# Optimization experiments

Measured on AMD Instinct MI355X. Metric: run time of the kernel, lower is better.

Reference implementation:

```python
import jax, jax.numpy as jnp
import numpy as np

N_NODES = 50000
N_EDGES = 800000
N_LABEL = 200000
IN_C, HID_C, OUT_C = 128, 128, 64


def setup_inputs() -> dict:
    key = jax.random.key(0)
    ks = jax.random.split(key, 9)
    s = lambda fan_in: 1.0 / np.sqrt(fan_in)
    return {
        "x": jax.random.normal(ks[0], (N_NODES, IN_C), jnp.float32),
        "W1": jax.random.normal(ks[1], (IN_C, HID_C), jnp.float32) * s(IN_C),
        "b1": jnp.zeros((HID_C,), jnp.float32),
        "W2": jax.random.normal(ks[2], (HID_C, HID_C), jnp.float32) * s(HID_C),
        "b2": jnp.zeros((HID_C,), jnp.float32),
        "W3": jax.random.normal(ks[3], (HID_C, OUT_C), jnp.float32) * s(HID_C),
        "b3": jnp.zeros((OUT_C,), jnp.float32),
        "edge_index": jax.random.randint(ks[4], (2, N_EDGES), 0, N_NODES, jnp.int32),
        "edge_label_index": jax.random.randint(ks[5], (2, N_LABEL), 0, N_NODES, jnp.int32),
    }


def _gcn_conv(x, W, b, src, dst, dinv, num_nodes):
    # x @ W then symmetric-normalized scatter-sum over edges (self-loops included in src/dst)
    h = x @ W                                  # [N, out]
    norm = dinv[src] * dinv[dst]               # [E+N]
    msgs = h[src] * norm[:, None]              # [E+N, out]
    out = jax.ops.segment_sum(msgs, dst, num_segments=num_nodes)
    return out + b


def _encode(x, W1, b1, W2, b2, W3, b3, edge_index, num_nodes):
    loops = jnp.arange(num_nodes, dtype=edge_index.dtype)
    src = jnp.concatenate([edge_index[0], loops])
    dst = jnp.concatenate([edge_index[1], loops])
    # degree (with self-loops) at targets; deg >= 1 so rsqrt is safe
    deg = jax.ops.segment_sum(jnp.ones(dst.shape[0], x.dtype), dst, num_segments=num_nodes)
    dinv = jax.lax.rsqrt(deg)
    z = _gcn_conv(x, W1, b1, src, dst, dinv, num_nodes)
    z = jax.nn.relu(z)  # dropout treated as eval-mode identity
    z = _gcn_conv(z, W2, b2, src, dst, dinv, num_nodes)
    z = jax.nn.relu(z)
    z = _gcn_conv(z, W3, b3, src, dst, dinv, num_nodes)
    return z


def reference(x, W1, b1, W2, b2, W3, b3, edge_index, edge_label_index):
    z = _encode(x, W1, b1, W2, b2, W3, b3, edge_index, N_NODES)
    # decode: gather both endpoints, elementwise mul, sum over feature dim
    return (z[edge_label_index[0]] * z[edge_label_index[1]]).sum(axis=-1)
```

## Files before the change

kernel.cpp:

```cpp
#include <hip/hip_runtime.h>

#define N_NODES 50000
#define N_EDGES 800000
#define N_LABEL 200000
#define ROW_BLOCKS 782

typedef __attribute__((ext_vector_type(4))) float f32x4;
typedef _Float16 f16;
typedef __attribute__((ext_vector_type(8))) _Float16 f16x8;

__global__ __launch_bounds__(256)
void k_zero(int4* __restrict__ p, int n4) {
    int i = blockIdx.x * 256 + threadIdx.x;
    if (i < n4) p[i] = int4{0, 0, 0, 0};
}

__global__ __launch_bounds__(256)
void k_prep(const float* __restrict__ W1, const float* __restrict__ W2,
            const float* __restrict__ W3,
            f16* WT1h, f16* WT1l, f16* WT2h, f16* WT2l, f16* WT3h, f16* WT3l,
            const int* __restrict__ dst, int* cnt) {
    int b = blockIdx.x, tid = threadIdx.x;
    if (b < 64) {
        int t = b * 256 + tid;
        int c = t >> 7, k = t & 127;
        float w = W1[k * 128 + c];
        f16 h = (f16)w;
        WT1h[c * 128 + k] = h; WT1l[c * 128 + k] = (f16)(w - (float)h);
        w = W2[k * 128 + c];
        h = (f16)w;
        WT2h[c * 128 + k] = h; WT2l[c * 128 + k] = (f16)(w - (float)h);
        if (c < 64) {
            w = W3[k * 64 + c];
            h = (f16)w;
            WT3h[c * 128 + k] = h; WT3l[c * 128 + k] = (f16)(w - (float)h);
        }
    } else {
        int vb = b - 64;
        int g = vb & 7;
        int i = (vb >> 3) * 256 + tid;
        int d = dst[i];
        if ((unsigned)(d - g * 6250) < 6250u) atomicAdd(&cnt[d], 1);
    }
}

__global__ __launch_bounds__(256)
void k_partial(const int* __restrict__ cnt, float* __restrict__ dinv,
               int* __restrict__ bsum, int N) {
    __shared__ int wsum[4];
    int b = blockIdx.x, t = threadIdx.x;
    int i = b * 256 + t;
    int v = (i < N) ? cnt[i] : 0;
    if (i < N) dinv[i] = rsqrtf((float)v + 1.0f);
    int s = v;
#pragma unroll
    for (int d = 1; d < 64; d <<= 1) s += __shfl_xor(s, d, 64);
    if ((t & 63) == 0) wsum[t >> 6] = s;
    __syncthreads();
    if (t == 0) bsum[b] = wsum[0] + wsum[1] + wsum[2] + wsum[3];
}

__global__ __launch_bounds__(256)
void k_offsets(const int* __restrict__ cnt, const int* __restrict__ bsum,
               int* __restrict__ off, int N, int NB) {
    __shared__ int wsum[4];
    __shared__ int add0_s;
    int b = blockIdx.x, t = threadIdx.x;
    int v0 = (t < b && t < NB) ? bsum[t] : 0;
    int s0 = v0;
#pragma unroll
    for (int d = 1; d < 64; d <<= 1) s0 += __shfl_xor(s0, d, 64);
    if ((t & 63) == 0) wsum[t >> 6] = s0;
    __syncthreads();
    if (t == 0) add0_s = wsum[0] + wsum[1] + wsum[2] + wsum[3];
    __syncthreads();
    int add = add0_s;
    __syncthreads();
    int i = b * 256 + t;
    int v = (i < N) ? cnt[i] : 0;
    int lane = t & 63, w = t >> 6;
    int sv = v;
#pragma unroll
    for (int d = 1; d < 64; d <<= 1) {
        int u = __shfl_up(sv, d, 64);
        if (lane >= d) sv += u;
    }
    if (lane == 63) wsum[w] = sv;
    __syncthreads();
    for (int ww = 0; ww < w; ++ww) add += wsum[ww];
    if (i < N) off[i + 1] = add + sv;
    if (i == 0) off[0] = 0;
}

__global__ __launch_bounds__(256)
void k_bucket(const int* __restrict__ srcv, const int* __restrict__ dstv,
              const int* __restrict__ off, int* cnt2, unsigned short* __restrict__ csr) {
    int vb = blockIdx.x;
    int g = vb & 7;
    int i = (vb >> 3) * 256 + threadIdx.x;
    int d = dstv[i];
    if ((unsigned)(d - g * 6250) < 6250u) {
        int slot = off[d] + atomicAdd(&cnt2[d], 1);
        csr[slot] = (unsigned short)srcv[i];
    }
}

__global__ __launch_bounds__(256)
void k_gemm1(const float* __restrict__ x,
             const f16* __restrict__ WTh, const f16* __restrict__ WTl,
             const float* __restrict__ dinv, f16* __restrict__ A, int N) {
    constexpr int M = 128, NCB = 4;
    __shared__ f16 Hs[64 * 136];
    __shared__ f16 Ls[64 * 136];
    int b = blockIdx.x;
    int c0 = (b & 1) * 64;
    int t = threadIdx.x;

#pragma unroll
    for (int i = 0; i < 4; ++i) {
        int ch = t + i * 256;
        int col = ch >> 4;
        int kc = (ch & 15) * 8;
        *(f16x8*)&Hs[col * 136 + kc] = *(const f16x8*)&WTh[(long)(c0 + col) * 128 + kc];
        *(f16x8*)&Ls[col * 136 + kc] = *(const f16x8*)&WTl[(long)(c0 + col) * 128 + kc];
    }

    int wv = t >> 6, l = t & 63;
    int r0w = (b >> 1) * 64 + wv * 16;
    int arow = r0w + (l & 15);
    if (arow >= N) arow = N - 1;
    int kb = (l >> 4) * 8;

    f16x8 ah[4], al[4];
#pragma unroll
    for (int ks = 0; ks < 4; ++ks) {
        const float* xp = &x[(long)arow * 128 + ks * 32 + kb];
        float4 a0 = *(const float4*)xp;
        float4 a1 = *(const float4*)(xp + 4);
        float fv[8] = {a0.x, a0.y, a0.z, a0.w, a1.x, a1.y, a1.z, a1.w};
#pragma unroll
        for (int j = 0; j < 8; ++j) {
            f16 h = (f16)fv[j];
            ah[ks][j] = h;
            al[ks][j] = (f16)(fv[j] - (float)h);
        }
    }
    __syncthreads();

    f32x4 acc[NCB];
#pragma unroll
    for (int cb = 0; cb < NCB; ++cb) acc[cb] = f32x4{0.f, 0.f, 0.f, 0.f};
#pragma unroll
    for (int ks = 0; ks < 4; ++ks) {
#pragma unroll
        for (int cb = 0; cb < NCB; ++cb) {
            int wi = (cb * 16 + (l & 15)) * 136 + ks * 32 + kb;
            f16x8 bh = *(const f16x8*)&Hs[wi];
            f16x8 bl = *(const f16x8*)&Ls[wi];
            acc[cb] = __builtin_amdgcn_mfma_f32_16x16x32_f16(ah[ks], bh, acc[cb], 0, 0, 0);
            acc[cb] = __builtin_amdgcn_mfma_f32_16x16x32_f16(ah[ks], bl, acc[cb], 0, 0, 0);
            acc[cb] = __builtin_amdgcn_mfma_f32_16x16x32_f16(al[ks], bh, acc[cb], 0, 0, 0);
        }
    }
    int rbase = r0w + (l >> 4) * 4;
    float dv[4];
#pragma unroll
    for (int i = 0; i < 4; ++i) dv[i] = (rbase + i < N) ? dinv[rbase + i] : 0.f;
#pragma unroll
    for (int cb = 0; cb < NCB; ++cb) {
#pragma unroll
        for (int i = 0; i < 4; ++i) {
            int r = rbase + i;
            if (r < N) A[(long)r * M + c0 + cb * 16 + (l & 15)] = (f16)(acc[cb][i] * dv[i]);
        }
    }
}

template<int M>
__global__ __launch_bounds__(256)
void k_gemm23(const f16* __restrict__ B,
              const f16* __restrict__ WTh, const f16* __restrict__ WTl,
              const float* __restrict__ dinv, f16* __restrict__ A, int N) {
    constexpr int NCB = M / 32;
    constexpr int HC = M / 2;
    __shared__ f16 Hs[HC * 136];
    __shared__ f16 Ls[HC * 136];
    int b = blockIdx.x;
    int c0 = (b & 1) * HC;
    int t = threadIdx.x;

#pragma unroll
    for (int i = 0; i < HC / 16; ++i) {
        int ch = t + i * 256;
        int col = ch >> 4;
        int kc = (ch & 15) * 8;
        *(f16x8*)&Hs[col * 136 + kc] = *(const f16x8*)&WTh[(long)(c0 + col) * 128 + kc];
        *(f16x8*)&Ls[col * 136 + kc] = *(const f16x8*)&WTl[(long)(c0 + col) * 128 + kc];
    }

    int wv = t >> 6, l = t & 63;
    int r0w = (b >> 1) * 64 + wv * 16;
    int arow = r0w + (l & 15);
    if (arow >= N) arow = N - 1;
    int kb = (l >> 4) * 8;

    f16x8 a[4];
#pragma unroll
    for (int ks = 0; ks < 4; ++ks)
        a[ks] = *(const f16x8*)&B[(long)arow * 128 + ks * 32 + kb];
    __syncthreads();

    f32x4 acc[NCB];
#pragma unroll
    for (int cb = 0; cb < NCB; ++cb) acc[cb] = f32x4{0.f, 0.f, 0.f, 0.f};
#pragma unroll
    for (int ks = 0; ks < 4; ++ks) {
#pragma unroll
        for (int cb = 0; cb < NCB; ++cb) {
            int wi = (cb * 16 + (l & 15)) * 136 + ks * 32 + kb;
            f16x8 bh = *(const f16x8*)&Hs[wi];
            f16x8 bl = *(const f16x8*)&Ls[wi];
            acc[cb] = __builtin_amdgcn_mfma_f32_16x16x32_f16(a[ks], bh, acc[cb], 0, 0, 0);
            acc[cb] = __builtin_amdgcn_mfma_f32_16x16x32_f16(a[ks], bl, acc[cb], 0, 0, 0);
        }
    }
    int rbase = r0w + (l >> 4) * 4;
    float dv[4];
#pragma unroll
    for (int i = 0; i < 4; ++i) dv[i] = (rbase + i < N) ? dinv[rbase + i] : 0.f;
#pragma unroll
    for (int cb = 0; cb < NCB; ++cb) {
#pragma unroll
        for (int i = 0; i < 4; ++i) {
            int r = rbase + i;
            if (r < N) A[(long)r * M + c0 + cb * 16 + (l & 15)] = (f16)(acc[cb][i] * dv[i]);
        }
    }
}

__global__ __launch_bounds__(256)
void k_gather(const f16* __restrict__ A, const int* __restrict__ off,
              const unsigned short* __restrict__ csr, const float* __restrict__ dinv,
              const float* __restrict__ bias, float* __restrict__ Bf,
              f16* __restrict__ Bo,
              int N, int M, int lg, int relu, int mode) {
    int t = blockIdx.x * blockDim.x + threadIdx.x;
    int node = t >> lg;
    if (node >= N) return;
    int q = (t & ((1 << lg) - 1)) << 3;
    const f16* Aq = A + q;

    float acc[8];
    {
        f16x8 v = *(const f16x8*)&Aq[(long)node * M];
#pragma unroll
        for (int c = 0; c < 8; ++c) acc[c] = (float)v[c];
    }
    int j = off[node], j1 = off[node + 1];
    for (; j + 8 <= j1; j += 8) {
        int s0 = csr[j + 0], s1 = csr[j + 1], s2 = csr[j + 2], s3 = csr[j + 3];
        int s4 = csr[j + 4], s5 = csr[j + 5], s6 = csr[j + 6], s7 = csr[j + 7];
        f16x8 v0 = *(const f16x8*)&Aq[(long)s0 * M];
        f16x8 v1 = *(const f16x8*)&Aq[(long)s1 * M];
        f16x8 v2 = *(const f16x8*)&Aq[(long)s2 * M];
        f16x8 v3 = *(const f16x8*)&Aq[(long)s3 * M];
        f16x8 v4 = *(const f16x8*)&Aq[(long)s4 * M];
        f16x8 v5 = *(const f16x8*)&Aq[(long)s5 * M];
        f16x8 v6 = *(const f16x8*)&Aq[(long)s6 * M];
        f16x8 v7 = *(const f16x8*)&Aq[(long)s7 * M];
#pragma unroll
        for (int c = 0; c < 8; ++c)
            acc[c] += ((float)v0[c] + (float)v1[c] + (float)v2[c] + (float)v3[c])
                    + ((float)v4[c] + (float)v5[c] + (float)v6[c] + (float)v7[c]);
    }
    for (; j + 2 <= j1; j += 2) {
        int s0 = csr[j + 0], s1 = csr[j + 1];
        f16x8 v0 = *(const f16x8*)&Aq[(long)s0 * M];
        f16x8 v1 = *(const f16x8*)&Aq[(long)s1 * M];
#pragma unroll
        for (int c = 0; c < 8; ++c) acc[c] += (float)v0[c] + (float)v1[c];
    }
    if (j < j1) {
        int s = csr[j];
        f16x8 v = *(const f16x8*)&Aq[(long)s * M];
#pragma unroll
        for (int c = 0; c < 8; ++c) acc[c] += (float)v[c];
    }

    float sc = dinv[node];
    float4 bb0 = *(const float4*)&bias[q];
    float4 bb1 = *(const float4*)&bias[q + 4];
    float bv[8] = {bb0.x, bb0.y, bb0.z, bb0.w, bb1.x, bb1.y, bb1.z, bb1.w};
#pragma unroll
    for (int c = 0; c < 8; ++c) {
        acc[c] = acc[c] * sc + bv[c];
        if (relu) acc[c] = fmaxf(acc[c], 0.f);
    }
    if (mode == 0) {
        float4 o0 = make_float4(acc[0], acc[1], acc[2], acc[3]);
        float4 o1 = make_float4(acc[4], acc[5], acc[6], acc[7]);
        *(float4*)&Bf[(long)node * M + q] = o0;
        *(float4*)&Bf[(long)node * M + q + 4] = o1;
    } else {
        f16x8 o;
#pragma unroll
        for (int c = 0; c < 8; ++c) o[c] = (f16)acc[c];
        *(f16x8*)&Bo[(long)node * M + q] = o;
    }
}

__global__ void k_decode(const float* __restrict__ z, const int* __restrict__ eli,
                         float* __restrict__ out, int L) {
    int t = blockIdx.x * blockDim.x + threadIdx.x;
    int e = t >> 4;
    int lane = t & 15;
    if (e >= L) return;
    int a = eli[e], b = eli[L + e];
    float4 va = *(const float4*)&z[(long)a * 64 + lane * 4];
    float4 vb = *(const float4*)&z[(long)b * 64 + lane * 4];
    float s = va.x * vb.x + va.y * vb.y + va.z * vb.z + va.w * vb.w;
    s += __shfl_xor(s, 1, 16);
    s += __shfl_xor(s, 2, 16);
    s += __shfl_xor(s, 4, 16);
    s += __shfl_xor(s, 8, 16);
    if (lane == 0) out[e] = s;
}

extern "C" void kernel_launch(void* const* d_in, const int* in_sizes, int n_in,
                              void* d_out, int out_size, void* d_ws, size_t ws_size,
                              hipStream_t stream) {
    const float* x   = (const float*)d_in[0];
    const float* W1  = (const float*)d_in[1];
    const float* b1  = (const float*)d_in[2];
    const float* W2  = (const float*)d_in[3];
    const float* b2  = (const float*)d_in[4];
    const float* W3  = (const float*)d_in[5];
    const float* b3  = (const float*)d_in[6];
    const int*   ei  = (const int*)d_in[7];
    const int*   eli = (const int*)d_in[8];
    float* out = (float*)d_out;

    char* ws = (char*)d_ws;
    float* dinv = (float*)ws;                  ws += 50048 * 4;
    f16*   A    = (f16*)ws;                    ws += (long)N_NODES * 128 * 2;
    f16*   B    = (f16*)ws;                    ws += (long)N_NODES * 128 * 2;
    float* z    = (float*)ws;                  ws += (long)N_NODES * 64 * 4;
    int*   cnt  = (int*)ws;                    ws += 50048 * 4;
    int*   cnt2 = (int*)ws;                    ws += 50048 * 4;
    int*   off  = (int*)ws;                    ws += 50048 * 4;
    unsigned short* csr = (unsigned short*)ws; ws += (long)N_EDGES * 2;
    int*   bsum = (int*)ws;                    ws += 256 * 4;
    f16*   WT1h = (f16*)ws;                    ws += 16384 * 2;
    f16*   WT1l = (f16*)ws;                    ws += 16384 * 2;
    f16*   WT2h = (f16*)ws;                    ws += 16384 * 2;
    f16*   WT2l = (f16*)ws;                    ws += 16384 * 2;
    f16*   WT3h = (f16*)ws;                    ws += 8192 * 2;
    f16*   WT3l = (f16*)ws;                    ws += 8192 * 2;

    const int* esrc = ei;
    const int* edst = ei + N_EDGES;

    const int NB = (N_NODES + 255) / 256;

    k_zero   <<<98, 256, 0, stream>>>((int4*)cnt, 25024);
    k_prep   <<<25064, 256, 0, stream>>>(W1, W2, W3, WT1h, WT1l, WT2h, WT2l,
                                         WT3h, WT3l, edst, cnt);
    k_partial<<<NB, 256, 0, stream>>>(cnt, dinv, bsum, N_NODES);
    k_offsets<<<NB, 256, 0, stream>>>(cnt, bsum, off, N_NODES, NB);
    k_bucket <<<25000, 256, 0, stream>>>(esrc, edst, off, cnt2, csr);

    const int ga128 = (N_NODES * 16 + 255) / 256;
    const int ga64  = (N_NODES * 8 + 255) / 256;

    k_gemm1<<<ROW_BLOCKS * 2, 256, 0, stream>>>(x, WT1h, WT1l, dinv, A, N_NODES);
    k_gather<<<ga128, 256, 0, stream>>>(A, off, csr, dinv, b1, nullptr, B,
                                        N_NODES, 128, 4, 1, 1);
    k_gemm23<128><<<ROW_BLOCKS * 2, 256, 0, stream>>>(B, WT2h, WT2l, dinv, A, N_NODES);
    k_gather<<<ga128, 256, 0, stream>>>(A, off, csr, dinv, b2, nullptr, B,
                                        N_NODES, 128, 4, 1, 1);
    k_gemm23<64><<<ROW_BLOCKS * 2, 256, 0, stream>>>(B, WT3h, WT3l, dinv, A, N_NODES);
    k_gather<<<ga64, 256, 0, stream>>>(A, off, csr, dinv, b3, z, nullptr,
                                       N_NODES, 64, 3, 0, 0);

    k_decode<<<(N_LABEL * 16 + 255) / 256, 256, 0, stream>>>(z, eli, out, N_LABEL);
}
```

Before: 216.8 us.

## Partition gather and decode work by XCD column slices for L2 locality

Gather kernels are specialized to fixed widths and remap block indices so each group of blocks (blockIdx mod 8) handles one column slice of the feature matrix and one node range. With round-robin block dispatch across XCDs, each XCD's L2 then only needs to cache a fraction of the gathered rows. Decode is likewise split into per-column-slice partial dot products written to a scratch buffer, then reduced by a second kernel. This adds an extra kernel launch and a 3.2 MB scratch buffer, and it relies on the hardware's block-to-XCD scheduling.

New measurement: 247.3 us. +14.0%, slower.

```diff
diff --git a/kernel.cpp b/kernel.cpp
--- a/kernel.cpp
+++ b/kernel.cpp
@@ -239,20 +239,21 @@
 }
 
 __global__ __launch_bounds__(256)
-void k_gather(const f16* __restrict__ A, const int* __restrict__ off,
-              const unsigned short* __restrict__ csr, const float* __restrict__ dinv,
-              const float* __restrict__ bias, float* __restrict__ Bf,
-              f16* __restrict__ Bo,
-              int N, int M, int lg, int relu, int mode) {
-    int t = blockIdx.x * blockDim.x + threadIdx.x;
-    int node = t >> lg;
-    if (node >= N) return;
-    int q = (t & ((1 << lg) - 1)) << 3;
+void k_gather128(const f16* __restrict__ A, const int* __restrict__ off,
+                 const unsigned short* __restrict__ csr, const float* __restrict__ dinv,
+                 const float* __restrict__ bias, f16* __restrict__ Bo) {
+    int vb = blockIdx.x;
+    int g = vb & 7, blk = vb >> 3;
+    int t = threadIdx.x;
+    int nl = blk * 64 + (t >> 2);
+    if (nl >= 25000) return;
+    int node = (g & 1) * 25000 + nl;
+    int q = (g >> 1) * 32 + (t & 3) * 8;
     const f16* Aq = A + q;
 
     float acc[8];
     {
-        f16x8 v = *(const f16x8*)&Aq[(long)node * M];
+        f16x8 v = *(const f16x8*)&Aq[(long)node * 128];
 #pragma unroll
         for (int c = 0; c < 8; ++c) acc[c] = (float)v[c];
     }
@@ -260,14 +261,14 @@
     for (; j + 8 <= j1; j += 8) {
         int s0 = csr[j + 0], s1 = csr[j + 1], s2 = csr[j + 2], s3 = csr[j + 3];
         int s4 = csr[j + 4], s5 = csr[j + 5], s6 = csr[j + 6], s7 = csr[j + 7];
-        f16x8 v0 = *(const f16x8*)&Aq[(long)s0 * M];
-        f16x8 v1 = *(const f16x8*)&Aq[(long)s1 * M];
-        f16x8 v2 = *(const f16x8*)&Aq[(long)s2 * M];
-        f16x8 v3 = *(const f16x8*)&Aq[(long)s3 * M];
-        f16x8 v4 = *(const f16x8*)&Aq[(long)s4 * M];
-        f16x8 v5 = *(const f16x8*)&Aq[(long)s5 * M];
-        f16x8 v6 = *(const f16x8*)&Aq[(long)s6 * M];
-        f16x8 v7 = *(const f16x8*)&Aq[(long)s7 * M];
+        f16x8 v0 = *(const f16x8*)&Aq[(long)s0 * 128];
+        f16x8 v1 = *(const f16x8*)&Aq[(long)s1 * 128];
+        f16x8 v2 = *(const f16x8*)&Aq[(long)s2 * 128];
+        f16x8 v3 = *(const f16x8*)&Aq[(long)s3 * 128];
+        f16x8 v4 = *(const f16x8*)&Aq[(long)s4 * 128];
+        f16x8 v5 = *(const f16x8*)&Aq[(long)s5 * 128];
+        f16x8 v6 = *(const f16x8*)&Aq[(long)s6 * 128];
+        f16x8 v7 = *(const f16x8*)&Aq[(long)s7 * 128];
 #pragma unroll
         for (int c = 0; c < 8; ++c)
             acc[c] += ((float)v0[c] + (float)v1[c] + (float)v2[c] + (float)v3[c])
@@ -275,55 +276,114 @@
     }
     for (; j + 2 <= j1; j += 2) {
         int s0 = csr[j + 0], s1 = csr[j + 1];
-        f16x8 v0 = *(const f16x8*)&Aq[(long)s0 * M];
-        f16x8 v1 = *(const f16x8*)&Aq[(long)s1 * M];
+        f16x8 v0 = *(const f16x8*)&Aq[(long)s0 * 128];
+        f16x8 v1 = *(const f16x8*)&Aq[(long)s1 * 128];
 #pragma unroll
         for (int c = 0; c < 8; ++c) acc[c] += (float)v0[c] + (float)v1[c];
     }
     if (j < j1) {
         int s = csr[j];
-        f16x8 v = *(const f16x8*)&Aq[(long)s * M];
+        f16x8 v = *(const f16x8*)&Aq[(long)s * 128];
 #pragma unroll
         for (int c = 0; c < 8; ++c) acc[c] += (float)v[c];
     }
-
     float sc = dinv[node];
     float4 bb0 = *(const float4*)&bias[q];
     float4 bb1 = *(const float4*)&bias[q + 4];
     float bv[8] = {bb0.x, bb0.y, bb0.z, bb0.w, bb1.x, bb1.y, bb1.z, bb1.w};
-#pragma unroll
-    for (int c = 0; c < 8; ++c) {
-        acc[c] = acc[c] * sc + bv[c];
-        if (relu) acc[c] = fmaxf(acc[c], 0.f);
-    }
-    if (mode == 0) {
-        float4 o0 = make_float4(acc[0], acc[1], acc[2], acc[3]);
-        float4 o1 = make_float4(acc[4], acc[5], acc[6], acc[7]);
-        *(float4*)&Bf[(long)node * M + q] = o0;
-        *(float4*)&Bf[(long)node * M + q + 4] = o1;
-    } else {
-        f16x8 o;
-#pragma unroll
-        for (int c = 0; c < 8; ++c) o[c] = (f16)acc[c];
-        *(f16x8*)&Bo[(long)node * M + q] = o;
-    }
-}
-
-__global__ void k_decode(const float* __restrict__ z, const int* __restrict__ eli,
-                         float* __restrict__ out, int L) {
-    int t = blockIdx.x * blockDim.x + threadIdx.x;
-    int e = t >> 4;
-    int lane = t & 15;
-    if (e >= L) return;
-    int a = eli[e], b = eli[L + e];
-    float4 va = *(const float4*)&z[(long)a * 64 + lane * 4];
-    float4 vb = *(const float4*)&z[(long)b * 64 + lane * 4];
-    float s = va.x * vb.x + va.y * vb.y + va.z * vb.z + va.w * vb.w;
-    s += __shfl_xor(s, 1, 16);
-    s += __shfl_xor(s, 2, 16);
-    s += __shfl_xor(s, 4, 16);
-    s += __shfl_xor(s, 8, 16);
-    if (lane == 0) out[e] = s;
+    f16x8 o;
+#pragma unroll
+    for (int c = 0; c < 8; ++c) o[c] = (f16)fmaxf(acc[c] * sc + bv[c], 0.f);
+    *(f16x8*)&Bo[(long)node * 128 + q] = o;
+}
+
+__global__ __launch_bounds__(256)
+void k_gather64(const f16* __restrict__ A, const int* __restrict__ off,
+                const unsigned short* __restrict__ csr, const float* __restrict__ dinv,
+                const float* __restrict__ bias, float* __restrict__ z) {
+    int vb = blockIdx.x;
+    int g = vb & 7, blk = vb >> 3;
+    int t = threadIdx.x;
+    int nl = blk * 64 + (t >> 2);
+    if (nl >= 12500) return;
+    int node = (g >> 1) * 12500 + nl;
+    int q = (g & 1) * 32 + (t & 3) * 8;
+    const f16* Aq = A + q;
+
+    float acc[8];
+    {
+        f16x8 v = *(const f16x8*)&Aq[(long)node * 64];
+#pragma unroll
+        for (int c = 0; c < 8; ++c) acc[c] = (float)v[c];
+    }
+    int j = off[node], j1 = off[node + 1];
+    for (; j + 8 <= j1; j += 8) {
+        int s0 = csr[j + 0], s1 = csr[j + 1], s2 = csr[j + 2], s3 = csr[j + 3];
+        int s4 = csr[j + 4], s5 = csr[j + 5], s6 = csr[j + 6], s7 = csr[j + 7];
+        f16x8 v0 = *(const f16x8*)&Aq[(long)s0 * 64];
+        f16x8 v1 = *(const f16x8*)&Aq[(long)s1 * 64];
+        f16x8 v2 = *(const f16x8*)&Aq[(long)s2 * 64];
+        f16x8 v3 = *(const f16x8*)&Aq[(long)s3 * 64];
+        f16x8 v4 = *(const f16x8*)&Aq[(long)s4 * 64];
+        f16x8 v5 = *(const f16x8*)&Aq[(long)s5 * 64];
+        f16x8 v6 = *(const f16x8*)&Aq[(long)s6 * 64];
+        f16x8 v7 = *(const f16x8*)&Aq[(long)s7 * 64];
+#pragma unroll
+        for (int c = 0; c < 8; ++c)
+            acc[c] += ((float)v0[c] + (float)v1[c] + (float)v2[c] + (float)v3[c])
+                    + ((float)v4[c] + (float)v5[c] + (float)v6[c] + (float)v7[c]);
+    }
+    for (; j + 2 <= j1; j += 2) {
+        int s0 = csr[j + 0], s1 = csr[j + 1];
+        f16x8 v0 = *(const f16x8*)&Aq[(long)s0 * 64];
+        f16x8 v1 = *(const f16x8*)&Aq[(long)s1 * 64];
+#pragma unroll
+        for (int c = 0; c < 8; ++c) acc[c] += (float)v0[c] + (float)v1[c];
+    }
+    if (j < j1) {
+        int s = csr[j];
+        f16x8 v = *(const f16x8*)&Aq[(long)s * 64];
+#pragma unroll
+        for (int c = 0; c < 8; ++c) acc[c] += (float)v[c];
+    }
+    float sc = dinv[node];
+    float4 bb0 = *(const float4*)&bias[q];
+    float4 bb1 = *(const float4*)&bias[q + 4];
+    float4 o0, o1;
+    o0.x = acc[0] * sc + bb0.x; o0.y = acc[1] * sc + bb0.y;
+    o0.z = acc[2] * sc + bb0.z; o0.w = acc[3] * sc + bb0.w;
+    o1.x = acc[4] * sc + bb1.x; o1.y = acc[5] * sc + bb1.y;
+    o1.z = acc[6] * sc + bb1.z; o1.w = acc[7] * sc + bb1.w;
+    *(float4*)&z[(long)node * 64 + q] = o0;
+    *(float4*)&z[(long)node * 64 + q + 4] = o1;
+}
+
+__global__ __launch_bounds__(256)
+void k_decode_part(const float* __restrict__ z, const int* __restrict__ eli,
+                   float* __restrict__ P) {
+    int vb = blockIdx.x;
+    int g = vb & 7, blk = vb >> 3;
+    int el = blk * 256 + threadIdx.x;
+    if (el >= 100000) return;
+    int e = (g & 1) * 100000 + el;
+    int cs = g >> 1;
+    const float* za = &z[(long)eli[e] * 64 + cs * 16];
+    const float* zb = &z[(long)eli[N_LABEL + e] * 64 + cs * 16];
+    float s = 0.f;
+#pragma unroll
+    for (int i = 0; i < 4; ++i) {
+        float4 a = *(const float4*)&za[i * 4];
+        float4 b = *(const float4*)&zb[i * 4];
+        s += a.x * b.x + a.y * b.y + a.z * b.z + a.w * b.w;
+    }
+    P[cs * N_LABEL + e] = s;
+}
+
+__global__ __launch_bounds__(256)
+void k_decode_red(const float* __restrict__ P, float* __restrict__ out) {
+    int e = blockIdx.x * 256 + threadIdx.x;
+    if (e < N_LABEL)
+        out[e] = (P[e] + P[N_LABEL + e]) + (P[2 * N_LABEL + e] + P[3 * N_LABEL + e]);
 }
 
 extern "C" void kernel_launch(void* const* d_in, const int* in_sizes, int n_in,
@@ -345,6 +405,7 @@
     f16*   A    = (f16*)ws;                    ws += (long)N_NODES * 128 * 2;
     f16*   B    = (f16*)ws;                    ws += (long)N_NODES * 128 * 2;
     float* z    = (float*)ws;                  ws += (long)N_NODES * 64 * 4;
+    float* P    = (float*)ws;                  ws += (long)4 * N_LABEL * 4;
     int*   cnt  = (int*)ws;                    ws += 50048 * 4;
     int*   cnt2 = (int*)ws;                    ws += 50048 * 4;
     int*   off  = (int*)ws;                    ws += 50048 * 4;
@@ -369,18 +430,13 @@
     k_offsets<<<NB, 256, 0, stream>>>(cnt, bsum, off, N_NODES, NB);
     k_bucket <<<25000, 256, 0, stream>>>(esrc, edst, off, cnt2, csr);
 
-    const int ga128 = (N_NODES * 16 + 255) / 256;
-    const int ga64  = (N_NODES * 8 + 255) / 256;
-
     k_gemm1<<<ROW_BLOCKS * 2, 256, 0, stream>>>(x, WT1h, WT1l, dinv, A, N_NODES);
-    k_gather<<<ga128, 256, 0, stream>>>(A, off, csr, dinv, b1, nullptr, B,
-                                        N_NODES, 128, 4, 1, 1);
+    k_gather128<<<391 * 8, 256, 0, stream>>>(A, off, csr, dinv, b1, B);
     k_gemm23<128><<<ROW_BLOCKS * 2, 256, 0, stream>>>(B, WT2h, WT2l, dinv, A, N_NODES);
-    k_gather<<<ga128, 256, 0, stream>>>(A, off, csr, dinv, b2, nullptr, B,
-                                        N_NODES, 128, 4, 1, 1);
+    k_gather128<<<391 * 8, 256, 0, stream>>>(A, off, csr, dinv, b2, B);
     k_gemm23<64><<<ROW_BLOCKS * 2, 256, 0, stream>>>(B, WT3h, WT3l, dinv, A, N_NODES);
-    k_gather<<<ga64, 256, 0, stream>>>(A, off, csr, dinv, b3, z, nullptr,
-                                       N_NODES, 64, 3, 0, 0);
-
-    k_decode<<<(N_LABEL * 16 + 255) / 256, 256, 0, stream>>>(z, eli, out, N_LABEL);
-}
+    k_gather64<<<196 * 8, 256, 0, stream>>>(A, off, csr, dinv, b3, z);
+
+    k_decode_part<<<391 * 8, 256, 0, stream>>>(z, eli, P);
+    k_decode_red <<<(N_LABEL + 255) / 256, 256, 0, stream>>>(P, out);
+}
```
